# Performance work log

Hardware: AMD Instinct MI355X
Metric: run time of the kernel (lower is better)

The kernel has to match this reference:

```python
import jax, jax.numpy as jnp
import numpy as np

B, P, D = 64, 128, 128   # clouds, points per cloud, vec_dim
N = B * P                # 8192 nodes
EPS = 1e-5


def _complete_graph_edges():
    # knn_graph with k == total node count => complete graph per cloud (no self loops)
    i = np.arange(P)
    ii, jj = np.meshgrid(i, i, indexing='ij')
    m = ii != jj
    li, lj = ii[m], jj[m]                      # [P*(P-1)] local pairs
    off = (np.arange(B) * P)[:, None]          # cloud offsets
    src = (off + li[None, :]).reshape(-1)      # neighbor index
    dst = (off + lj[None, :]).reshape(-1)      # center index
    return jnp.asarray(src, jnp.int32), jnp.asarray(dst, jnp.int32)


def setup_inputs() -> dict:
    key = jax.random.key(0)
    ks = jax.random.split(key, 4)
    src, dst = _complete_graph_edges()
    return {
        'x': jax.random.normal(ks[0], (N, D), jnp.float32),
        'xyz': jax.random.normal(ks[1], (N, 3), jnp.float32),
        'W_xyz': jax.random.normal(ks[2], (3, D), jnp.float32) * 0.1,
        'bn_gamma': jnp.ones((D,), jnp.float32),
        'bn_beta': jnp.zeros((D,), jnp.float32),
        'W1': jax.random.normal(ks[3], (D, D), jnp.float32) * 0.05,
        'b1': jnp.zeros((D,), jnp.float32),
        'ln_gamma': jnp.ones((D,), jnp.float32),
        'ln_beta': jnp.zeros((D,), jnp.float32),
        'src': src,
        'dst': dst,
    }


def reference(x, xyz, W_xyz, bn_gamma, bn_beta, W1, b1, ln_gamma, ln_beta, src, dst):
    n = x.shape[0]
    rela_xyz = xyz[src] - xyz[dst]                         # [E, 3]
    rela_x = x[src] - x[dst]                               # [E, D]
    dist = jnp.sqrt(jnp.sum(rela_xyz * rela_xyz, axis=-1))  # [E]
    w = jnp.exp(-dist)[:, None]                            # [E, 1]

    # weighted linear + relu, pool by src (global_add_pool over node index)
    h1 = jax.nn.relu((w * rela_x) @ W1 + b1)               # [E, D]
    p1 = jax.ops.segment_sum(h1, src, num_segments=n)      # [N, D]
    mu = jnp.mean(p1, axis=-1, keepdims=True)
    var = jnp.var(p1, axis=-1, keepdims=True)
    x = x + ((p1 - mu) / jnp.sqrt(var + EPS)) * ln_gamma + ln_beta

    # xyz projection branch, BatchNorm1d (training-mode batch stats)
    h2 = jax.nn.relu(rela_xyz @ W_xyz)                     # [E, D]
    p2 = jax.ops.segment_sum(h2, src, num_segments=n)      # [N, D]
    bmu = jnp.mean(p2, axis=0)
    bvar = jnp.var(p2, axis=0)
    x = x + ((p2 - bmu) / jnp.sqrt(bvar + EPS)) * bn_gamma + bn_beta
    return x
```

## Files before the change

kernel.cpp:

```cpp
#include <hip/hip_runtime.h>
#include <stdint.h>

#define EPS 1e-5f
#define N_NODES 8192

typedef __attribute__((ext_vector_type(8))) short short8;
typedef __attribute__((ext_vector_type(4))) float floatx4;
typedef __attribute__((ext_vector_type(2))) float floatx2;
typedef __attribute__((ext_vector_type(4))) unsigned short ushortx4;

__device__ __forceinline__ unsigned short f2bf(float f) {
    uint32_t u = __float_as_uint(f);
    u += 0x7FFFu + ((u >> 16) & 1u);
    return (unsigned short)(u >> 16);
}

__global__ __launch_bounds__(256) void prep_kernel(
    const float* __restrict__ x, const float* __restrict__ W1,
    const float* __restrict__ xyz,
    unsigned short* __restrict__ xb, unsigned short* __restrict__ w1t,
    float* __restrict__ xyz4, float* __restrict__ stat_ws)
{
    const int bx = blockIdx.x, tid = threadIdx.x;
    if (bx < 1024) {
        const int base = bx * 1024 + tid * 4;
        floatx4 v = *(const floatx4*)(x + base);
        ushortx4 o = { f2bf(v[0]), f2bf(v[1]), f2bf(v[2]), f2bf(v[3]) };
        *(ushortx4*)(xb + base) = o;
    } else if (bx < 1040) {
        const int b2 = bx - 1024;
        const int n = b2 * 8 + (tid >> 5);
        const int k = (tid & 31) * 4;
#pragma unroll
        for (int e = 0; e < 4; ++e)
            w1t[n * 128 + k + e] = f2bf(W1[(k + e) * 128 + n]);
        if (b2 == 0) {
            floatx4 z = {0.f, 0.f, 0.f, 0.f};
            *(floatx4*)(stat_ws + tid * 4) = z;
        }
    } else {
        const int node = (bx - 1040) * 1024 + tid * 4;
#pragma unroll
        for (int e = 0; e < 4; ++e) {
            const float* p = xyz + (node + e) * 3;
            floatx4 v = { p[0], p[1], p[2], 0.f };
            *(floatx4*)(xyz4 + (node + e) * 4) = v;
        }
    }
}

__global__ __launch_bounds__(64) void gemm_yz_kernel(
    const unsigned short* __restrict__ xb, const unsigned short* __restrict__ w1t,
    const float* __restrict__ xyz4, const float* __restrict__ W_xyz,
    float* __restrict__ yz)
{
    const int lane = threadIdx.x;
    const int ml = lane & 15, q = lane >> 4;
    const int rb = blockIdx.x * 16;

    short8 afrag[4];
#pragma unroll
    for (int c = 0; c < 4; ++c)
        afrag[c] = *(const short8*)(xb + (rb + ml) * 128 + c * 32 + q * 8);

    floatx4 xn[4];
#pragma unroll
    for (int r = 0; r < 4; ++r)
        xn[r] = *(const floatx4*)(xyz4 + (rb + q * 4 + r) * 4);

#pragma unroll
    for (int nt = 0; nt < 8; ++nt) {
        const int ncol = nt * 16 + ml;
        const float wx0 = W_xyz[ncol], wx1 = W_xyz[128 + ncol], wx2 = W_xyz[256 + ncol];
        floatx4 acc = {0.f, 0.f, 0.f, 0.f};
#pragma unroll
        for (int c = 0; c < 4; ++c) {
            short8 b = *(const short8*)(w1t + ncol * 128 + c * 32 + q * 8);
            acc = __builtin_amdgcn_mfma_f32_16x16x32_bf16(afrag[c], b, acc, 0, 0, 0);
        }
#pragma unroll
        for (int r = 0; r < 4; ++r) {
            const int node = rb + q * 4 + r;
            float zv = xn[r][0] * wx0 + xn[r][1] * wx1 + xn[r][2] * wx2;
            floatx2 st = { acc[r], zv };
            *(floatx2*)(yz + node * 256 + 2 * ncol) = st;
        }
    }
}

__global__ __launch_bounds__(256, 4) void cloud_main_kernel(
    const float* __restrict__ x, const float* __restrict__ b1,
    const float* __restrict__ ln_gamma, const float* __restrict__ ln_beta,
    const float* __restrict__ xyz4, const float* __restrict__ yz,
    float* __restrict__ p2_ws, float* __restrict__ stat_ws,
    float* __restrict__ out)
{
    __shared__ float s_xyz[512];
    __shared__ float s_w[1024];
    __shared__ float s_red[2048];
    __shared__ float s_p1[1088];
    __shared__ float s_bn[256];
    __shared__ float s_mu[8];
    __shared__ float s_rs[8];

    const int bx = blockIdx.x;
    const int c = bx & 63, s = bx >> 6;
    const int tid = threadIdx.x;
    const int d = tid & 127, h = tid >> 7;
    const int node0 = c * 128;
    const int i0 = s * 8;

    if (tid < 128)
        *(floatx4*)(s_xyz + tid * 4) = *(const floatx4*)(xyz4 + (node0 + tid) * 4);
    __syncthreads();

    for (int e = tid; e < 1024; e += 256) {
        const int j = e >> 3, ii = e & 7, ia = i0 + ii;
        float dx = s_xyz[ia * 4]     - s_xyz[j * 4];
        float dy = s_xyz[ia * 4 + 1] - s_xyz[j * 4 + 1];
        float dz = s_xyz[ia * 4 + 2] - s_xyz[j * 4 + 2];
        s_w[j * 8 + ii] = __expf(-sqrtf(dx * dx + dy * dy + dz * dz));
    }
    __syncthreads();

    const float b1d = b1[d];
    const floatx2 b1v = {b1d, b1d};
    const floatx2 zv2 = {0.f, 0.f};

    const float* __restrict__ yzrow = yz + node0 * 256 + 2 * d;

    floatx2 yi[4], zi[4], a1[4], a2[4];
#pragma unroll
    for (int r = 0; r < 8; ++r) {
        floatx2 v = *(const floatx2*)(yzrow + (i0 + r) * 256);
        yi[r >> 1][r & 1] = v[0];
        zi[r >> 1][r & 1] = v[1];
        a1[r >> 1][r & 1] = 0.f;
        a2[r >> 1][r & 1] = 0.f;
    }

    const float* __restrict__ yzp = yzrow + h * 64 * 256;
    const float* __restrict__ wp = s_w + h * 64 * 8;

#pragma unroll 4
    for (int jj = 0; jj < 64; ++jj) {
        floatx2 yzj = *(const floatx2*)(yzp + jj * 256);
        floatx4 wa = *(const floatx4*)(wp + jj * 8);
        floatx4 wb = *(const floatx4*)(wp + jj * 8 + 4);
        const floatx2 yj2 = {yzj[0], yzj[0]}, zj2 = {yzj[1], yzj[1]};
        floatx2 w01 = {wa[0], wa[1]}, w23 = {wa[2], wa[3]};
        floatx2 w45 = {wb[0], wb[1]}, w67 = {wb[2], wb[3]};
        a1[0] += __builtin_elementwise_max(w01 * (yi[0] - yj2) + b1v, zv2);
        a1[1] += __builtin_elementwise_max(w23 * (yi[1] - yj2) + b1v, zv2);
        a1[2] += __builtin_elementwise_max(w45 * (yi[2] - yj2) + b1v, zv2);
        a1[3] += __builtin_elementwise_max(w67 * (yi[3] - yj2) + b1v, zv2);
        a2[0] += __builtin_elementwise_max(zi[0] - zj2, zv2);
        a2[1] += __builtin_elementwise_max(zi[1] - zj2, zv2);
        a2[2] += __builtin_elementwise_max(zi[2] - zj2, zv2);
        a2[3] += __builtin_elementwise_max(zi[3] - zj2, zv2);
    }

    if (h == 1) {
#pragma unroll
        for (int r = 0; r < 8; ++r) {
            s_red[r * 128 + d]        = a1[r >> 1][r & 1];
            s_red[1024 + r * 128 + d] = a2[r >> 1][r & 1];
        }
    }
    __syncthreads();

    if (h == 0) {
        const float selfc = fmaxf(b1d, 0.f);
        float bs = 0.f, bq = 0.f;
#pragma unroll
        for (int r = 0; r < 8; ++r) {
            float v1 = a1[r >> 1][r & 1] + s_red[r * 128 + d] - selfc;
            float v2 = a2[r >> 1][r & 1] + s_red[1024 + r * 128 + d];
            a1[r >> 1][r & 1] = v1;
            a2[r >> 1][r & 1] = v2;
            s_p1[r * 136 + d] = v1;
            bs += v2;
            bq += v2 * v2;
        }
        s_bn[d] = bs;
        s_bn[128 + d] = bq;
    }
    __syncthreads();

    {
        const int ii = tid >> 5, sub = tid & 31;
        floatx4 v = *(const floatx4*)(s_p1 + ii * 136 + sub * 4);
        float ps = v[0] + v[1] + v[2] + v[3];
        float pq = v[0] * v[0] + v[1] * v[1] + v[2] * v[2] + v[3] * v[3];
#pragma unroll
        for (int m = 1; m < 32; m <<= 1) {
            ps += __shfl_xor(ps, m, 64);
            pq += __shfl_xor(pq, m, 64);
        }
        if (sub == 0) {
            float mu = ps * (1.f / 128.f);
            float var = pq * (1.f / 128.f) - mu * mu;
            s_mu[ii] = mu;
            s_rs[ii] = rsqrtf(var + EPS);
        }
    }
    if (tid < 128) {
        const int bank = (s & 3) * 256;
        atomicAdd(stat_ws + bank + d,       s_bn[d]);
        atomicAdd(stat_ws + bank + 128 + d, s_bn[128 + d]);
    }
    __syncthreads();

    if (h == 0) {
        const float lng = ln_gamma[d], lnb = ln_beta[d];
#pragma unroll
        for (int r = 0; r < 8; ++r) {
            const int gi = node0 + i0 + r;
            float o = x[gi * 128 + d] + (a1[r >> 1][r & 1] - s_mu[r]) * s_rs[r] * lng + lnb;
            out[gi * 128 + d] = o;
            p2_ws[gi * 128 + d] = a2[r >> 1][r & 1];
        }
    }
}

__global__ __launch_bounds__(256) void finalize_kernel(
    const float* __restrict__ p2_ws, const float* __restrict__ stat_ws,
    const float* __restrict__ bn_gamma, const float* __restrict__ bn_beta,
    float* __restrict__ out)
{
    __shared__ float sA[128], sB[128];
    const int tid = threadIdx.x;
    if (tid < 128) {
        float sm = 0.f, sq = 0.f;
#pragma unroll
        for (int b = 0; b < 4; ++b) {
            sm += stat_ws[b * 256 + tid];
            sq += stat_ws[b * 256 + 128 + tid];
        }
        float mu = sm * (1.f / 8192.f);
        float var = sq * (1.f / 8192.f) - mu * mu;
        float rs = rsqrtf(var + EPS);
        float A = rs * bn_gamma[tid];
        sA[tid] = A;
        sB[tid] = bn_beta[tid] - mu * A;
    }
    __syncthreads();
    const int base = (blockIdx.x * 256 + tid) * 4;
    const int d0 = base & 127;
    floatx4 p2 = *(const floatx4*)(p2_ws + base);
    floatx4 o  = *(const floatx4*)(out + base);
#pragma unroll
    for (int e = 0; e < 4; ++e)
        o[e] += p2[e] * sA[d0 + e] + sB[d0 + e];
    *(floatx4*)(out + base) = o;
}

extern "C" void kernel_launch(void* const* d_in, const int* in_sizes, int n_in,
                              void* d_out, int out_size, void* d_ws, size_t ws_size,
                              hipStream_t stream) {
    const float* x        = (const float*)d_in[0];
    const float* xyz      = (const float*)d_in[1];
    const float* W_xyz    = (const float*)d_in[2];
    const float* bn_gamma = (const float*)d_in[3];
    const float* bn_beta  = (const float*)d_in[4];
    const float* W1       = (const float*)d_in[5];
    const float* b1       = (const float*)d_in[6];
    const float* ln_gamma = (const float*)d_in[7];
    const float* ln_beta  = (const float*)d_in[8];
    float* out = (float*)d_out;

    float* yz_ws   = (float*)d_ws;
    float* p2_ws   = yz_ws + N_NODES * 256;
    float* stat_ws = p2_ws + N_NODES * 128;
    unsigned short* xb  = (unsigned short*)(stat_ws + 1024);
    unsigned short* w1t = xb + N_NODES * 128;
    float* xyz4 = (float*)(w1t + 128 * 128);

    prep_kernel<<<1048, 256, 0, stream>>>(x, W1, xyz, xb, w1t, xyz4, stat_ws);
    gemm_yz_kernel<<<512, 64, 0, stream>>>(xb, w1t, xyz4, W_xyz, yz_ws);
    cloud_main_kernel<<<1024, 256, 0, stream>>>(x, b1, ln_gamma, ln_beta,
                                                xyz4, yz_ws, p2_ws, stat_ws, out);
    finalize_kernel<<<1024, 256, 0, stream>>>(p2_ws, stat_ws, bn_gamma, bn_beta, out);
}
```

Baseline: 114.3 us.

## Use packed-f32 inline asm in pairwise loop and spread BN stat atomics over 16 banks

The inner pairwise loop of the cloud kernel now uses inline v_pk_add_f32 with op_sel to subtract a splatted neighbour value, plus v_pk_fma_f32, so no separate splat moves are needed. The ReLU accumulations become scalar fmaxf adds on separate lo/hi accumulators. Separately, BatchNorm statistic atomics are spread over 16 banks instead of 4 to cut atomic contention, with the workspace and the finalize reduction enlarged to match. The inline asm limits compiler scheduling, and the scalar max/add may offset the gain from the packed ops.

```diff
diff --git a/kernel.cpp b/kernel.cpp
--- a/kernel.cpp
+++ b/kernel.cpp
@@ -13,6 +13,24 @@
     uint32_t u = __float_as_uint(f);
     u += 0x7FFFu + ((u >> 16) & 1u);
     return (unsigned short)(u >> 16);
+}
+
+__device__ __forceinline__ floatx2 pk_sub_splat_lo(floatx2 a, floatx2 b) {
+    floatx2 d;
+    asm("v_pk_add_f32 %0, %1, %2 op_sel:[0,0] op_sel_hi:[1,0] neg_lo:[0,1] neg_hi:[0,1]"
+        : "=v"(d) : "v"(a), "v"(b));
+    return d;
+}
+__device__ __forceinline__ floatx2 pk_sub_splat_hi(floatx2 a, floatx2 b) {
+    floatx2 d;
+    asm("v_pk_add_f32 %0, %1, %2 op_sel:[0,1] op_sel_hi:[1,1] neg_lo:[0,1] neg_hi:[0,1]"
+        : "=v"(d) : "v"(a), "v"(b));
+    return d;
+}
+__device__ __forceinline__ floatx2 pk_fma(floatx2 a, floatx2 b, floatx2 c) {
+    floatx2 d;
+    asm("v_pk_fma_f32 %0, %1, %2, %3" : "=v"(d) : "v"(a), "v"(b), "v"(c));
+    return d;
 }
 
 __global__ __launch_bounds__(256) void prep_kernel(
@@ -34,9 +52,9 @@
 #pragma unroll
         for (int e = 0; e < 4; ++e)
             w1t[n * 128 + k + e] = f2bf(W1[(k + e) * 128 + n]);
-        if (b2 == 0) {
+        if (b2 < 4) {
             floatx4 z = {0.f, 0.f, 0.f, 0.f};
-            *(floatx4*)(stat_ws + tid * 4) = z;
+            *(floatx4*)(stat_ws + b2 * 1024 + tid * 4) = z;
         }
     } else {
         const int node = (bx - 1040) * 1024 + tid * 4;
@@ -125,19 +143,19 @@
 
     const float b1d = b1[d];
     const floatx2 b1v = {b1d, b1d};
-    const floatx2 zv2 = {0.f, 0.f};
 
     const float* __restrict__ yzrow = yz + node0 * 256 + 2 * d;
 
-    floatx2 yi[4], zi[4], a1[4], a2[4];
+    floatx2 yi[4], zi[4];
+    float a1l[4], a1h[4], a2l[4], a2h[4];
 #pragma unroll
     for (int r = 0; r < 8; ++r) {
         floatx2 v = *(const floatx2*)(yzrow + (i0 + r) * 256);
         yi[r >> 1][r & 1] = v[0];
         zi[r >> 1][r & 1] = v[1];
-        a1[r >> 1][r & 1] = 0.f;
-        a2[r >> 1][r & 1] = 0.f;
-    }
+    }
+#pragma unroll
+    for (int p = 0; p < 4; ++p) { a1l[p] = a1h[p] = a2l[p] = a2h[p] = 0.f; }
 
     const float* __restrict__ yzp = yzrow + h * 64 * 256;
     const float* __restrict__ wp = s_w + h * 64 * 8;
@@ -147,40 +165,42 @@
         floatx2 yzj = *(const floatx2*)(yzp + jj * 256);
         floatx4 wa = *(const floatx4*)(wp + jj * 8);
         floatx4 wb = *(const floatx4*)(wp + jj * 8 + 4);
-        const floatx2 yj2 = {yzj[0], yzj[0]}, zj2 = {yzj[1], yzj[1]};
-        floatx2 w01 = {wa[0], wa[1]}, w23 = {wa[2], wa[3]};
-        floatx2 w45 = {wb[0], wb[1]}, w67 = {wb[2], wb[3]};
-        a1[0] += __builtin_elementwise_max(w01 * (yi[0] - yj2) + b1v, zv2);
-        a1[1] += __builtin_elementwise_max(w23 * (yi[1] - yj2) + b1v, zv2);
-        a1[2] += __builtin_elementwise_max(w45 * (yi[2] - yj2) + b1v, zv2);
-        a1[3] += __builtin_elementwise_max(w67 * (yi[3] - yj2) + b1v, zv2);
-        a2[0] += __builtin_elementwise_max(zi[0] - zj2, zv2);
-        a2[1] += __builtin_elementwise_max(zi[1] - zj2, zv2);
-        a2[2] += __builtin_elementwise_max(zi[2] - zj2, zv2);
-        a2[3] += __builtin_elementwise_max(zi[3] - zj2, zv2);
+        floatx2 wpr[4] = { {wa[0], wa[1]}, {wa[2], wa[3]},
+                           {wb[0], wb[1]}, {wb[2], wb[3]} };
+#pragma unroll
+        for (int p = 0; p < 4; ++p) {
+            floatx2 dy = pk_sub_splat_lo(yi[p], yzj);
+            floatx2 t  = pk_fma(wpr[p], dy, b1v);
+            a1l[p] += fmaxf(t[0], 0.f);
+            a1h[p] += fmaxf(t[1], 0.f);
+            floatx2 dz = pk_sub_splat_hi(zi[p], yzj);
+            a2l[p] += fmaxf(dz[0], 0.f);
+            a2h[p] += fmaxf(dz[1], 0.f);
+        }
     }
 
     if (h == 1) {
 #pragma unroll
         for (int r = 0; r < 8; ++r) {
-            s_red[r * 128 + d]        = a1[r >> 1][r & 1];
-            s_red[1024 + r * 128 + d] = a2[r >> 1][r & 1];
-        }
-    }
-    __syncthreads();
-
+            s_red[r * 128 + d]        = (r & 1) ? a1h[r >> 1] : a1l[r >> 1];
+            s_red[1024 + r * 128 + d] = (r & 1) ? a2h[r >> 1] : a2l[r >> 1];
+        }
+    }
+    __syncthreads();
+
+    float m1[8], m2[8];
     if (h == 0) {
         const float selfc = fmaxf(b1d, 0.f);
         float bs = 0.f, bq = 0.f;
 #pragma unroll
         for (int r = 0; r < 8; ++r) {
-            float v1 = a1[r >> 1][r & 1] + s_red[r * 128 + d] - selfc;
-            float v2 = a2[r >> 1][r & 1] + s_red[1024 + r * 128 + d];
-            a1[r >> 1][r & 1] = v1;
-            a2[r >> 1][r & 1] = v2;
-            s_p1[r * 136 + d] = v1;
-            bs += v2;
-            bq += v2 * v2;
+            float p1v = ((r & 1) ? a1h[r >> 1] : a1l[r >> 1]) + s_red[r * 128 + d] - selfc;
+            float p2v = ((r & 1) ? a2h[r >> 1] : a2l[r >> 1]) + s_red[1024 + r * 128 + d];
+            m1[r] = p1v;
+            m2[r] = p2v;
+            s_p1[r * 136 + d] = p1v;
+            bs += p2v;
+            bq += p2v * p2v;
         }
         s_bn[d] = bs;
         s_bn[128 + d] = bq;
@@ -205,7 +225,7 @@
         }
     }
     if (tid < 128) {
-        const int bank = (s & 3) * 256;
+        const int bank = s * 256;
         atomicAdd(stat_ws + bank + d,       s_bn[d]);
         atomicAdd(stat_ws + bank + 128 + d, s_bn[128 + d]);
     }
@@ -216,9 +236,9 @@
 #pragma unroll
         for (int r = 0; r < 8; ++r) {
             const int gi = node0 + i0 + r;
-            float o = x[gi * 128 + d] + (a1[r >> 1][r & 1] - s_mu[r]) * s_rs[r] * lng + lnb;
+            float o = x[gi * 128 + d] + (m1[r] - s_mu[r]) * s_rs[r] * lng + lnb;
             out[gi * 128 + d] = o;
-            p2_ws[gi * 128 + d] = a2[r >> 1][r & 1];
+            p2_ws[gi * 128 + d] = m2[r];
         }
     }
 }
@@ -233,7 +253,7 @@
     if (tid < 128) {
         float sm = 0.f, sq = 0.f;
 #pragma unroll
-        for (int b = 0; b < 4; ++b) {
+        for (int b = 0; b < 16; ++b) {
             sm += stat_ws[b * 256 + tid];
             sq += stat_ws[b * 256 + 128 + tid];
         }
@@ -272,7 +292,7 @@
     float* yz_ws   = (float*)d_ws;
     float* p2_ws   = yz_ws + N_NODES * 256;
     float* stat_ws = p2_ws + N_NODES * 128;
-    unsigned short* xb  = (unsigned short*)(stat_ws + 1024);
+    unsigned short* xb  = (unsigned short*)(stat_ws + 4096);
     unsigned short* w1t = xb + N_NODES * 128;
     float* xyz4 = (float*)(w1t + 128 * 128);
 
```

After: 120.4 us. 1.05x slower.
